# Optimization experiments

Hardware: AMD Instinct MI355X
Metric: run time of the kernel (lower is better)

The kernel has to match this reference:

```python
import jax, jax.numpy as jnp
import numpy as np


def setup_inputs() -> dict:
    key = jax.random.key(0)
    k1, k2 = jax.random.split(key)
    lut = jax.random.normal(k1, (1, 3, 33, 33, 33), dtype=jnp.float32)
    x = jax.random.uniform(k2, (8, 3, 1024, 1024), dtype=jnp.float32)
    return {"lut": lut, "x": x}


def reference(lut, x):
    # lut: [1, 3, D, D, D]; x: [B, 3, H, W] in [0,1]
    D = lut.shape[-1]
    lut0 = lut[0]  # [3, D, D, D], broadcast over batch (lut batch == 1)

    v = jnp.clip(x, 0.0, 1.0) * (D - 1)            # [B, 3, H, W]
    v = jnp.transpose(v, (0, 2, 3, 1))             # [B, H, W, 3]
    i0 = jnp.floor(v).astype(jnp.int32)            # [B, H, W, 3]
    i1 = jnp.minimum(i0 + 1, D - 1)
    f = v - i0.astype(v.dtype)                     # fractional part

    r0, g0, b0 = i0[..., 0], i0[..., 1], i0[..., 2]
    r1, g1, b1 = i1[..., 0], i1[..., 1], i1[..., 2]
    fr, fg, fb = f[..., 0], f[..., 1], f[..., 2]

    def gather(rr, gg, bb):
        # lut0[:, rr, gg, bb] -> [3, B, H, W] -> [B, 3, H, W]
        return jnp.transpose(lut0[:, rr, gg, bb], (1, 0, 2, 3))

    c000 = gather(r0, g0, b0)
    c100 = gather(r1, g0, b0)
    c010 = gather(r0, g1, b0)
    c110 = gather(r1, g1, b0)
    c001 = gather(r0, g0, b1)
    c101 = gather(r1, g0, b1)
    c011 = gather(r0, g1, b1)
    c111 = gather(r1, g1, b1)

    one = jnp.float32(1.0)
    w000 = ((one - fr) * (one - fg) * (one - fb))[:, None]
    w100 = (fr * (one - fg) * (one - fb))[:, None]
    w010 = ((one - fr) * fg * (one - fb))[:, None]
    w110 = (fr * fg * (one - fb))[:, None]
    w001 = ((one - fr) * (one - fg) * fb)[:, None]
    w101 = (fr * (one - fg) * fb)[:, None]
    w011 = ((one - fr) * fg * fb)[:, None]
    w111 = (fr * fg * fb)[:, None]

    out = (c000 * w000 + c100 * w100 + c010 * w010 + c110 * w110 +
           c001 * w001 + c101 * w101 + c011 * w011 + c111 * w111)
    return out  # [B, 3, H, W]
```

## Files before the change

kernel.cpp:

```cpp
#include <hip/hip_runtime.h>


#define D   33
#define D2  (33 * 33)
#define D3  (33 * 33 * 33)
#define HW  (1024 * 1024)
#define BATCH 8
#define QHW (HW / 4)
#define NG  (BATCH * QHW)
#define CHUNKS 256
#define GPC (NG / CHUNKS)
#define THREADS 1024

__global__ __launch_bounds__(THREADS) void lut3d_kernel(
    const float* __restrict__ lut, const float* __restrict__ x,
    float* __restrict__ out)
{
    const int c     = blockIdx.x;
    const int chunk = blockIdx.y;

    __shared__ float ls[D3];
    {
        const float* lc = lut + c * D3;
        for (int i = threadIdx.x; i < D3; i += THREADS) ls[i] = lc[i];
    }
    __syncthreads();

    const int tid  = threadIdx.x;
    const int base = chunk * GPC;

    #pragma unroll 1
    for (int it = 0; it < GPC / THREADS; ++it) {
        const int g = base + it * THREADS + tid;
        const int b = g >> 18;
        const int p = (g & (QHW - 1)) * 4;

        const float* xb = x + (size_t)b * 3 * HW + p;
        const float4 xr = *(const float4*)(xb);
        const float4 xg = *(const float4*)(xb + HW);
        const float4 xB = *(const float4*)(xb + 2 * HW);

        const float rr[4] = {xr.x, xr.y, xr.z, xr.w};
        const float gg[4] = {xg.x, xg.y, xg.z, xg.w};
        const float bb[4] = {xB.x, xB.y, xB.z, xB.w};
        float oo[4];

        #pragma unroll
        for (int j = 0; j < 4; ++j) {
            const float vr = fminf(fmaxf(rr[j], 0.f), 1.f) * 32.f;
            const float vg = fminf(fmaxf(gg[j], 0.f), 1.f) * 32.f;
            const float vb = fminf(fmaxf(bb[j], 0.f), 1.f) * 32.f;

            const float r0f = floorf(vr);
            const float g0f = floorf(vg);
            const float b0f = floorf(vb);
            const int r0 = (int)r0f, g0 = (int)g0f, b0 = (int)b0f;
            const float fr = vr - r0f, fg = vg - g0f, fb = vb - b0f;

            const int dr = (r0 < D - 1) ? D2 : 0;
            const int dg = (g0 < D - 1) ? D  : 0;
            const int db = (b0 < D - 1) ? 1  : 0;
            const int idx = r0 * D2 + g0 * D + b0;

            const float c000 = ls[idx];
            const float c001 = ls[idx + db];
            const float c010 = ls[idx + dg];
            const float c011 = ls[idx + dg + db];
            const float c100 = ls[idx + dr];
            const float c101 = ls[idx + dr + db];
            const float c110 = ls[idx + dr + dg];
            const float c111 = ls[idx + dr + dg + db];

            const float c00 = c000 + fb * (c001 - c000);
            const float c01 = c010 + fb * (c011 - c010);
            const float c10 = c100 + fb * (c101 - c100);
            const float c11 = c110 + fb * (c111 - c110);
            const float c0  = c00 + fg * (c01 - c00);
            const float c1  = c10 + fg * (c11 - c10);
            oo[j] = c0 + fr * (c1 - c0);
        }

        float* ob = out + (size_t)b * 3 * HW + (size_t)c * HW + p;
        *(float4*)ob = make_float4(oo[0], oo[1], oo[2], oo[3]);
    }
}

extern "C" void kernel_launch(void* const* d_in, const int* in_sizes, int n_in,
                              void* d_out, int out_size, void* d_ws, size_t ws_size,
                              hipStream_t stream) {
    const float* lut = (const float*)d_in[0];
    const float* x   = (const float*)d_in[1];
    float* out = (float*)d_out;

    dim3 grid(3, CHUNKS);
    lut3d_kernel<<<grid, THREADS, 0, stream>>>(lut, x, out);
}
```

Measured before the change: 212.7 us.

## Pack LUT neighbor pairs as half2 in LDS and remap blocks across XCDs

Each shared-memory entry now stores a half2 holding the LUT value and its b+1 neighbor, which halves the LDS reads per pixel from eight to four. Indices are clamped to D-2 so the neighbor offsets no longer need branches. Blocks are remapped so the three channels of the same chunk land on the same XCD, which lets them share x in L2, and outputs are written with nontemporal stores. Storing the LUT in fp16 lowers its precision, which may exceed the accuracy tolerance.

New measurement: 224.4 us. 1.05x slower.

```diff
diff --git a/kernel.cpp b/kernel.cpp
--- a/kernel.cpp
+++ b/kernel.cpp
@@ -1,4 +1,5 @@
 #include <hip/hip_runtime.h>
+#include <hip/hip_fp16.h>
 
 
 #define D   33
@@ -12,17 +13,28 @@
 #define GPC (NG / CHUNKS)
 #define THREADS 1024
 
+typedef float v4f __attribute__((ext_vector_type(4)));
+
 __global__ __launch_bounds__(THREADS) void lut3d_kernel(
     const float* __restrict__ lut, const float* __restrict__ x,
     float* __restrict__ out)
 {
-    const int c     = blockIdx.x;
-    const int chunk = blockIdx.y;
+    const int id    = blockIdx.x;
+    const int xcd   = id & 7;
+    const int slot  = id >> 3;
+    const int c     = slot % 3;
+    const int chunk = (slot / 3) * 8 + xcd;
 
-    __shared__ float ls[D3];
+    __shared__ __half2 ls[D3];
     {
         const float* lc = lut + c * D3;
-        for (int i = threadIdx.x; i < D3; i += THREADS) ls[i] = lc[i];
+        for (int i = threadIdx.x; i < D3; i += THREADS) {
+            const int q  = i / D;
+            const int b  = i - q * D;
+            const float v0 = lc[i];
+            const float v1 = (b < D - 1) ? lc[i + 1] : v0;
+            ls[i] = __floats2half2_rn(v0, v1);
+        }
     }
     __syncthreads();
 
@@ -36,52 +48,44 @@
         const int p = (g & (QHW - 1)) * 4;
 
         const float* xb = x + (size_t)b * 3 * HW + p;
-        const float4 xr = *(const float4*)(xb);
-        const float4 xg = *(const float4*)(xb + HW);
-        const float4 xB = *(const float4*)(xb + 2 * HW);
+        const v4f xr = *(const v4f*)(xb);
+        const v4f xg = *(const v4f*)(xb + HW);
+        const v4f xB = *(const v4f*)(xb + 2 * HW);
 
-        const float rr[4] = {xr.x, xr.y, xr.z, xr.w};
-        const float gg[4] = {xg.x, xg.y, xg.z, xg.w};
-        const float bb[4] = {xB.x, xB.y, xB.z, xB.w};
-        float oo[4];
+        v4f oo;
 
         #pragma unroll
         for (int j = 0; j < 4; ++j) {
-            const float vr = fminf(fmaxf(rr[j], 0.f), 1.f) * 32.f;
-            const float vg = fminf(fmaxf(gg[j], 0.f), 1.f) * 32.f;
-            const float vb = fminf(fmaxf(bb[j], 0.f), 1.f) * 32.f;
+            const float vr = fminf(fmaxf(xr[j], 0.f), 1.f) * 32.f;
+            const float vg = fminf(fmaxf(xg[j], 0.f), 1.f) * 32.f;
+            const float vb = fminf(fmaxf(xB[j], 0.f), 1.f) * 32.f;
 
-            const float r0f = floorf(vr);
-            const float g0f = floorf(vg);
-            const float b0f = floorf(vb);
-            const int r0 = (int)r0f, g0 = (int)g0f, b0 = (int)b0f;
-            const float fr = vr - r0f, fg = vg - g0f, fb = vb - b0f;
+            const int r0 = min((int)vr, D - 2);
+            const int g0 = min((int)vg, D - 2);
+            const int b0 = min((int)vb, D - 2);
+            const float fr = vr - (float)r0;
+            const float fg = vg - (float)g0;
+            const float fb = vb - (float)b0;
 
-            const int dr = (r0 < D - 1) ? D2 : 0;
-            const int dg = (g0 < D - 1) ? D  : 0;
-            const int db = (b0 < D - 1) ? 1  : 0;
             const int idx = r0 * D2 + g0 * D + b0;
 
-            const float c000 = ls[idx];
-            const float c001 = ls[idx + db];
-            const float c010 = ls[idx + dg];
-            const float c011 = ls[idx + dg + db];
-            const float c100 = ls[idx + dr];
-            const float c101 = ls[idx + dr + db];
-            const float c110 = ls[idx + dr + dg];
-            const float c111 = ls[idx + dr + dg + db];
+            const __half2 h00 = ls[idx];
+            const __half2 h01 = ls[idx + D];
+            const __half2 h10 = ls[idx + D2];
+            const __half2 h11 = ls[idx + D2 + D];
 
-            const float c00 = c000 + fb * (c001 - c000);
-            const float c01 = c010 + fb * (c011 - c010);
-            const float c10 = c100 + fb * (c101 - c100);
-            const float c11 = c110 + fb * (c111 - c110);
-            const float c0  = c00 + fg * (c01 - c00);
-            const float c1  = c10 + fg * (c11 - c10);
-            oo[j] = c0 + fr * (c1 - c0);
+            const float c00 = fmaf(fb, __high2float(h00) - __low2float(h00), __low2float(h00));
+            const float c01 = fmaf(fb, __high2float(h01) - __low2float(h01), __low2float(h01));
+            const float c10 = fmaf(fb, __high2float(h10) - __low2float(h10), __low2float(h10));
+            const float c11 = fmaf(fb, __high2float(h11) - __low2float(h11), __low2float(h11));
+
+            const float c0 = fmaf(fg, c01 - c00, c00);
+            const float c1 = fmaf(fg, c11 - c10, c10);
+            oo[j] = fmaf(fr, c1 - c0, c0);
         }
 
         float* ob = out + (size_t)b * 3 * HW + (size_t)c * HW + p;
-        *(float4*)ob = make_float4(oo[0], oo[1], oo[2], oo[3]);
+        __builtin_nontemporal_store(oo, (v4f*)ob);
     }
 }
 
@@ -92,6 +96,5 @@
     const float* x   = (const float*)d_in[1];
     float* out = (float*)d_out;
 
-    dim3 grid(3, CHUNKS);
-    lut3d_kernel<<<grid, THREADS, 0, stream>>>(lut, x, out);
+    lut3d_kernel<<<dim3(3 * CHUNKS), THREADS, 0, stream>>>(lut, x, out);
 }
```
